# Kernel tuning notes

Hardware: AMD Instinct MI355X
Metric: run time of the kernel (lower is better)

Reference implementation:

```python
import jax, jax.numpy as jnp
import numpy as np

D_MODEL = 1024
N_HEADS = 16
FEATURE_DIM = 16
HEAD_DIM = D_MODEL // N_HEADS  # 64
EPS = 1e-12


def taylor_exp(x):
    """2nd-order Taylor feature map of exp(q^T k / sqrt(d)).
    x: (b, h, l, d) -> (b, h, l, 1 + d + d^2)"""
    d = x.shape[-1]
    rd = jnp.sqrt(jnp.asarray(d, x.dtype))      # sqrt(d)
    rrd = jnp.sqrt(rd)                          # d^(1/4)
    r2 = jnp.sqrt(jnp.asarray(2.0, x.dtype))
    x2 = (x[..., :, None] * x[..., None, :]).reshape(*x.shape[:-1], d * d) / r2
    ones = jnp.ones_like(x[..., :1])
    return jnp.concatenate([ones, x / rrd, x2 / rd], axis=-1)


def setup_inputs() -> dict:
    key = jax.random.key(0)
    k0, k1, k2, k3, k4 = jax.random.split(key, 5)
    b, l = 1, 1024
    scale = 1.0 / np.sqrt(D_MODEL)
    hidden_states = jax.random.normal(k0, (b, l, D_MODEL), dtype=jnp.float32)
    Wq = jax.random.normal(k1, (N_HEADS * FEATURE_DIM, D_MODEL), dtype=jnp.float32) * scale
    Wk = jax.random.normal(k2, (N_HEADS * FEATURE_DIM, D_MODEL), dtype=jnp.float32) * scale
    Wv = jax.random.normal(k3, (N_HEADS * HEAD_DIM, D_MODEL), dtype=jnp.float32) * scale
    Wo = jax.random.normal(k4, (D_MODEL, N_HEADS * HEAD_DIM), dtype=jnp.float32) * scale
    return {"hidden_states": hidden_states, "Wq": Wq, "Wk": Wk, "Wv": Wv, "Wo": Wo}


def reference(hidden_states, Wq, Wk, Wv, Wo):
    b, l, _ = hidden_states.shape
    # projections (bias-free)
    q = (hidden_states @ Wq.T).reshape(b, l, N_HEADS, FEATURE_DIM).transpose(0, 2, 1, 3)
    k = (hidden_states @ Wk.T).reshape(b, l, N_HEADS, FEATURE_DIM).transpose(0, 2, 1, 3)
    v = (hidden_states @ Wv.T).reshape(b, l, N_HEADS, HEAD_DIM).transpose(0, 2, 1, 3)
    qf = taylor_exp(q)   # (b, h, l, D) with D = 1 + d + d^2 = 273
    kf = taylor_exp(k)
    # causal linear attention via associative KV accumulation
    # kv_state[l] = sum_{t<=l} phi(k_t) outer v_t  -> (b, h, l, head_dim, D)
    kv_state = jnp.cumsum(kf[..., None, :] * v[..., :, None], axis=2)
    num = jnp.einsum('bhlD,bhldD->bhld', qf, kv_state)
    den = jnp.einsum('bhlD,bhlD->bhl', qf, jnp.cumsum(kf, axis=2))[..., None] + EPS
    y = num / den                                # (b, h, l, head_dim)
    y = y.transpose(0, 2, 1, 3).reshape(b, l, N_HEADS * HEAD_DIM)
    return y @ Wo.T
```

## Files before the change

kernel.cpp:

```cpp
#include <hip/hip_runtime.h>

#define LSEQ 1024
#define DMODEL 1024
#define NHEADS 16
#define FDIM 16
#define HDIM 64
#define CHUNK 64
#define NCHUNK 16

typedef __attribute__((ext_vector_type(8))) short short8;
typedef __attribute__((ext_vector_type(4))) float floatx4;

__device__ __forceinline__ float bf2f(unsigned short u) {
    unsigned int x = ((unsigned int)u) << 16;
    return __builtin_bit_cast(float, x);
}
__device__ __forceinline__ unsigned short f2bf(float f) {
    unsigned int x = __builtin_bit_cast(unsigned int, f);
    unsigned int r = (x + 0x7fffu + ((x >> 16) & 1u)) >> 16;
    return (unsigned short)r;
}

__device__ __forceinline__ int block_detect_fp32(const unsigned short* wq) {
    __shared__ int cnt;
    if (threadIdx.x == 0) cnt = 0;
    __syncthreads();
    int bad = 0;
    for (int i = threadIdx.x; i < 1024; i += blockDim.x) {
        int e = (wq[i] >> 7) & 0xFF;
        if (e >= 143 || (e > 0 && e <= 80)) bad++;
    }
    if (bad) atomicAdd(&cnt, bad);
    __syncthreads();
    return cnt > 128;
}

#define U_QB   0
#define U_KB   262144
#define U_VB   524288
#define U_YB   1572864
#define U_END  2621440

#define MFMA(a, b, c) __builtin_amdgcn_mfma_f32_16x16x32_bf16((a), (b), (c), 0, 0, 0)

__device__ __forceinline__ void gemm64_body(
    unsigned short (&As)[64][136], unsigned short (&Bs)[64][136],
    const void* Araw, int a_fp32, int arow0,
    const void* Braw, int b_fp32, int brow0, floatx4 acc[4]) {
    int t = threadIdx.x;
    int r = t >> 2, c0 = (t & 3) * 32;
    int wave = t >> 6, lane = t & 63;
    int ml = lane & 15, q4 = lane >> 4;
    int mq = (wave >> 1) * 32, nq = (wave & 1) * 32;
    #pragma unroll
    for (int i = 0; i < 4; ++i) acc[i] = (floatx4){0.f, 0.f, 0.f, 0.f};

    short8 av[4], bv[4], av2[4], bv2[4];
    auto stage = [&](int k0, short8* a, short8* b) {
        if (!a_fp32) {
            const unsigned short* Ap = (const unsigned short*)Araw + (size_t)(arow0 + r) * DMODEL + k0 + c0;
            #pragma unroll
            for (int j = 0; j < 4; ++j) a[j] = *(const short8*)(Ap + j * 8);
        } else {
            const float* Ap = (const float*)Araw + (size_t)(arow0 + r) * DMODEL + k0 + c0;
            #pragma unroll
            for (int j = 0; j < 4; ++j) {
                float4 f0 = *(const float4*)(Ap + j * 8);
                float4 f1 = *(const float4*)(Ap + j * 8 + 4);
                short8 x;
                x[0] = (short)f2bf(f0.x); x[1] = (short)f2bf(f0.y);
                x[2] = (short)f2bf(f0.z); x[3] = (short)f2bf(f0.w);
                x[4] = (short)f2bf(f1.x); x[5] = (short)f2bf(f1.y);
                x[6] = (short)f2bf(f1.z); x[7] = (short)f2bf(f1.w);
                a[j] = x;
            }
        }
        if (!b_fp32) {
            const unsigned short* Bp = (const unsigned short*)Braw + (size_t)(brow0 + r) * DMODEL + k0 + c0;
            #pragma unroll
            for (int j = 0; j < 4; ++j) b[j] = *(const short8*)(Bp + j * 8);
        } else {
            const float* Bp = (const float*)Braw + (size_t)(brow0 + r) * DMODEL + k0 + c0;
            #pragma unroll
            for (int j = 0; j < 4; ++j) {
                float4 f0 = *(const float4*)(Bp + j * 8);
                float4 f1 = *(const float4*)(Bp + j * 8 + 4);
                short8 x;
                x[0] = (short)f2bf(f0.x); x[1] = (short)f2bf(f0.y);
                x[2] = (short)f2bf(f0.z); x[3] = (short)f2bf(f0.w);
                x[4] = (short)f2bf(f1.x); x[5] = (short)f2bf(f1.y);
                x[6] = (short)f2bf(f1.z); x[7] = (short)f2bf(f1.w);
                b[j] = x;
            }
        }
    };

    stage(0, av, bv);
    for (int k0 = 0; k0 < DMODEL; k0 += 128) {
        __syncthreads();
        #pragma unroll
        for (int j = 0; j < 4; ++j) {
            *(short8*)&As[r][c0 + j * 8] = av[j];
            *(short8*)&Bs[r][c0 + j * 8] = bv[j];
        }
        __syncthreads();
        if (k0 + 128 < DMODEL) stage(k0 + 128, av2, bv2);
        #pragma unroll
        for (int kk = 0; kk < 4; ++kk) {
            short8 a0 = *(const short8*)&As[mq + ml][kk * 32 + q4 * 8];
            short8 a1 = *(const short8*)&As[mq + 16 + ml][kk * 32 + q4 * 8];
            short8 b0 = *(const short8*)&Bs[nq + ml][kk * 32 + q4 * 8];
            short8 b1 = *(const short8*)&Bs[nq + 16 + ml][kk * 32 + q4 * 8];
            acc[0] = MFMA(a0, b0, acc[0]); acc[1] = MFMA(a0, b1, acc[1]);
            acc[2] = MFMA(a1, b0, acc[2]); acc[3] = MFMA(a1, b1, acc[3]);
        }
        #pragma unroll
        for (int j = 0; j < 4; ++j) { av[j] = av2[j]; bv[j] = bv2[j]; }
    }
}

__global__ __launch_bounds__(256) void qkv_gemm(
    const void* __restrict__ hidR, const void* __restrict__ WqR,
    const void* __restrict__ WkR, const void* __restrict__ WvR,
    unsigned short* __restrict__ qb, unsigned short* __restrict__ kb,
    unsigned short* __restrict__ vb) {
    int fp32 = block_detect_fp32((const unsigned short*)WqR);
    __shared__ __align__(16) unsigned short As[64][136];
    __shared__ __align__(16) unsigned short Bs[64][136];
    int nb = blockIdx.x, mb = blockIdx.y;
    const void* Braw; unsigned short* Cout; int ldc, col0, br0;
    if (nb < 4)      { Braw = WqR; br0 = nb * 64;       Cout = qb; ldc = 256;  col0 = nb * 64; }
    else if (nb < 8) { Braw = WkR; br0 = (nb - 4) * 64; Cout = kb; ldc = 256;  col0 = (nb - 4) * 64; }
    else             { Braw = WvR; br0 = (nb - 8) * 64; Cout = vb; ldc = 1024; col0 = (nb - 8) * 64; }

    floatx4 acc[4];
    gemm64_body(As, Bs, hidR, fp32, mb * 64, Braw, fp32, br0, acc);

    int wave = threadIdx.x >> 6, lane = threadIdx.x & 63;
    int ml = lane & 15, q4 = lane >> 4;
    int mq = (wave >> 1) * 32, nq = (wave & 1) * 32;
    #pragma unroll
    for (int mi = 0; mi < 2; ++mi)
        #pragma unroll
        for (int ni = 0; ni < 2; ++ni) {
            floatx4 a = acc[mi * 2 + ni];
            int nloc = nq + ni * 16 + ml;
            #pragma unroll
            for (int r4 = 0; r4 < 4; ++r4) {
                int row = mb * 64 + mq + mi * 16 + q4 * 4 + r4;
                Cout[(size_t)row * ldc + col0 + nloc] = f2bf(a[r4]);
            }
        }
}

__global__ __launch_bounds__(256) void flash_partial(
    const unsigned short* __restrict__ qb, const unsigned short* __restrict__ kb,
    const unsigned short* __restrict__ vb,
    float* __restrict__ numW, float* __restrict__ denW) {
    int idx = blockIdx.x & 255;
    int s = blockIdx.x >> 8;
    int h = idx & 15, c = idx >> 4;
    int half = (c + 1) >> 1;
    int j0 = s ? half : 0;
    int j1 = s ? c : half - 1;
    int l0 = c * CHUNK;
    __shared__ __align__(16) unsigned short qs[64][40];
    __shared__ __align__(16) unsigned short ksm[64][40];
    __shared__ __align__(16) unsigned short vT[80][72];
    __shared__ __align__(16) unsigned short P[64][72];
    int t = threadIdx.x, lane = t & 63, wave = t >> 6;
    int ml = lane & 15, q4 = lane >> 4;
    int m0 = wave * 16;
    int sm = t >> 2, si4 = (t & 3) * 4, scc = (t & 3) * 16;

    {
        *(ushort4*)&qs[sm][si4] = *(const ushort4*)&qb[(size_t)(l0 + sm) * 256 + h * 16 + si4];
        ushort4 z = {0, 0, 0, 0};
        *(ushort4*)&qs[sm][16 + si4]  = z;
        *(ushort4*)&ksm[sm][16 + si4] = z;
    }
    if (t < 64) {
        vT[64][t] = 0x3F80;
        #pragma unroll
        for (int i = 65; i < 80; ++i) vT[i][t] = 0;
    }

    auto load_kv = [&](int j, ushort4& kr, ushort4 vr[4]) {
        kr = *(const ushort4*)&kb[(size_t)(j * 64 + sm) * 256 + h * 16 + si4];
        #pragma unroll
        for (int u = 0; u < 4; ++u)
            vr[u] = *(const ushort4*)&vb[(size_t)(j * 64 + sm) * 1024 + h * 64 + scc + u * 4];
    };

    floatx4 acc[5];
    #pragma unroll
    for (int i = 0; i < 5; ++i) acc[i] = (floatx4){0.f, 0.f, 0.f, 0.f};

    ushort4 kr, vr[4], kr2, vr2[4];
    if (j0 <= j1) {
        load_kv(j0, kr, vr);
        for (int j = j0; j <= j1; ++j) {
            {
                *(ushort4*)&ksm[sm][si4] = kr;
                unsigned short tmp[16];
                #pragma unroll
                for (int u = 0; u < 4; ++u) *(ushort4*)&tmp[u * 4] = vr[u];
                #pragma unroll
                for (int u = 0; u < 16; ++u) vT[scc + u][sm] = tmp[u];
            }
            __syncthreads();
            if (j < j1) load_kv(j + 1, kr2, vr2);

            short8 aq = *(const short8*)&qs[m0 + ml][q4 * 8];
            bool diag = (j == c);
            #pragma unroll
            for (int nt = 0; nt < 4; ++nt) {
                short8 bk = *(const short8*)&ksm[nt * 16 + ml][q4 * 8];
                floatx4 s4 = {0.f, 0.f, 0.f, 0.f};
                s4 = MFMA(aq, bk, s4);
                int tt = nt * 16 + ml;
                #pragma unroll
                for (int r = 0; r < 4; ++r) {
                    int lrow = m0 + q4 * 4 + r;
                    float sc = s4[r];
                    float p = 1.f + 0.25f * sc + 0.03125f * sc * sc;
                    if (diag && tt > lrow) p = 0.f;
                    P[lrow][tt] = f2bf(p);
                }
            }

            #pragma unroll
            for (int k0 = 0; k0 < 64; k0 += 32) {
                short8 ap = *(const short8*)&P[m0 + ml][k0 + q4 * 8];
                #pragma unroll
                for (int nt = 0; nt < 5; ++nt) {
                    short8 bvv = *(const short8*)&vT[nt * 16 + ml][k0 + q4 * 8];
                    acc[nt] = MFMA(ap, bvv, acc[nt]);
                }
            }
            __syncthreads();
            kr = kr2;
            #pragma unroll
            for (int u = 0; u < 4; ++u) vr[u] = vr2[u];
        }
    }

    float* np = numW + ((size_t)idx * 2 + s) * 4096;
    #pragma unroll
    for (int nt = 0; nt < 4; ++nt)
        #pragma unroll
        for (int r = 0; r < 4; ++r)
            np[(m0 + q4 * 4 + r) * 64 + nt * 16 + ml] = acc[nt][r];
    if (ml == 0) {
        float* dp = denW + ((size_t)idx * 2 + s) * 64;
        #pragma unroll
        for (int r = 0; r < 4; ++r) dp[m0 + q4 * 4 + r] = acc[4][r];
    }
}

__global__ __launch_bounds__(256) void attn_combine(
    const float* __restrict__ numW, const float* __restrict__ denW,
    unsigned short* __restrict__ ybB) {
    int idx = blockIdx.x;
    int h = idx & 15, c = idx >> 4;
    int l0 = c * CHUNK;
    int t = threadIdx.x;
    int row = t >> 2, col0 = (t & 3) * 16;
    const float* n0 = numW + (size_t)idx * 2 * 4096 + row * 64 + col0;
    const float* n1 = n0 + 4096;
    const float* dp = denW + (size_t)idx * 2 * 64 + row;
    float den = dp[0] + dp[64] + 1e-12f;
    float dinv = 1.f / den;
    short8 o0, o1;
    #pragma unroll
    for (int u = 0; u < 8; ++u)  o0[u] = (short)f2bf((n0[u] + n1[u]) * dinv);
    #pragma unroll
    for (int u = 8; u < 16; ++u) o1[u - 8] = (short)f2bf((n0[u] + n1[u]) * dinv);
    unsigned short* yp = ybB + (size_t)(l0 + row) * 1024 + h * 64 + col0;
    *(short8*)yp       = o0;
    *(short8*)(yp + 8) = o1;
}

__global__ __launch_bounds__(256) void out_gemm(
    const unsigned short* __restrict__ A, const void* __restrict__ WoR,
    void* __restrict__ outv, const unsigned short* __restrict__ wqraw) {
    int fp32 = block_detect_fp32(wqraw);
    __shared__ __align__(16) unsigned short As[64][136];
    __shared__ __align__(16) unsigned short Bs[64][136];
    int nb = blockIdx.x, mb = blockIdx.y;

    floatx4 acc[4];
    gemm64_body(As, Bs, A, 0, mb * 64, WoR, fp32, nb * 64, acc);

    int wave = threadIdx.x >> 6, lane = threadIdx.x & 63;
    int ml = lane & 15, q4 = lane >> 4;
    int mq = (wave >> 1) * 32, nq = (wave & 1) * 32;
    #pragma unroll
    for (int mi = 0; mi < 2; ++mi)
        #pragma unroll
        for (int ni = 0; ni < 2; ++ni) {
            floatx4 a = acc[mi * 2 + ni];
            int n = nb * 64 + nq + ni * 16 + ml;
            #pragma unroll
            for (int r4 = 0; r4 < 4; ++r4) {
                int row = mb * 64 + mq + mi * 16 + q4 * 4 + r4;
                size_t idx = (size_t)row * 1024 + n;
                if (fp32) ((float*)outv)[idx] = a[r4];
                else      ((unsigned short*)outv)[idx] = f2bf(a[r4]);
            }
        }
}

extern "C" void kernel_launch(void* const* d_in, const int* in_sizes, int n_in,
                              void* d_out, int out_size, void* d_ws, size_t ws_size,
                              hipStream_t stream) {
    unsigned short* us = (unsigned short*)d_ws;
    unsigned short* qbB = us + U_QB;
    unsigned short* kbB = us + U_KB;
    unsigned short* vbB = us + U_VB;
    unsigned short* ybB = us + U_YB;
    float* fws  = (float*)(us + U_END);
    float* numW = fws;
    float* denW = fws + 2097152;
    size_t need = (size_t)U_END * 2ull + (size_t)(2097152 + 32768) * 4ull;
    if (ws_size < need) return;

    qkv_gemm<<<dim3(24, 16), 256, 0, stream>>>(d_in[0], d_in[1], d_in[2], d_in[3], qbB, kbB, vbB);
    flash_partial<<<dim3(512), 256, 0, stream>>>(qbB, kbB, vbB, numW, denW);
    attn_combine<<<dim3(256), 256, 0, stream>>>(numW, denW, ybB);
    out_gemm<<<dim3(16, 16), 256, 0, stream>>>(ybB, d_in[4], d_out, (const unsigned short*)d_in[1]);
}
```

Before: 140.0 us.

## Fuse attention combine into output GEMM and store V transposed

Removes the attn_combine kernel. The output GEMM now reads the two partial numerator and denominator buffers directly, normalizes them, converts to bf16 and stages them into its A tile. The QKV GEMM writes V transposed, so flash_partial can load it with vector loads instead of scattering a transpose into shared memory. The PV MFMA operands are swapped so accumulator results can be written out as float4, and the bf16 conversion now uses the native __bf16 cast. The trade-off is that the output GEMM reads fp32 partials twice over (16 column blocks each reread them) instead of a single bf16 Y buffer.

```diff
diff --git a/kernel.cpp b/kernel.cpp
--- a/kernel.cpp
+++ b/kernel.cpp
@@ -11,14 +11,8 @@
 typedef __attribute__((ext_vector_type(8))) short short8;
 typedef __attribute__((ext_vector_type(4))) float floatx4;
 
-__device__ __forceinline__ float bf2f(unsigned short u) {
-    unsigned int x = ((unsigned int)u) << 16;
-    return __builtin_bit_cast(float, x);
-}
 __device__ __forceinline__ unsigned short f2bf(float f) {
-    unsigned int x = __builtin_bit_cast(unsigned int, f);
-    unsigned int r = (x + 0x7fffu + ((x >> 16) & 1u)) >> 16;
-    return (unsigned short)r;
+    return __builtin_bit_cast(unsigned short, (__bf16)f);
 }
 
 __device__ __forceinline__ int block_detect_fp32(const unsigned short* wq) {
@@ -37,8 +31,7 @@
 
 #define U_QB   0
 #define U_KB   262144
-#define U_VB   524288
-#define U_YB   1572864
+#define U_VT   524288
 #define U_END  2621440
 
 #define MFMA(a, b, c) __builtin_amdgcn_mfma_f32_16x16x32_bf16((a), (b), (c), 0, 0, 0)
@@ -56,6 +49,14 @@
     for (int i = 0; i < 4; ++i) acc[i] = (floatx4){0.f, 0.f, 0.f, 0.f};
 
     short8 av[4], bv[4], av2[4], bv2[4];
+    auto cvt8 = [](float4 f0, float4 f1) {
+        short8 x;
+        x[0] = (short)f2bf(f0.x); x[1] = (short)f2bf(f0.y);
+        x[2] = (short)f2bf(f0.z); x[3] = (short)f2bf(f0.w);
+        x[4] = (short)f2bf(f1.x); x[5] = (short)f2bf(f1.y);
+        x[6] = (short)f2bf(f1.z); x[7] = (short)f2bf(f1.w);
+        return x;
+    };
     auto stage = [&](int k0, short8* a, short8* b) {
         if (!a_fp32) {
             const unsigned short* Ap = (const unsigned short*)Araw + (size_t)(arow0 + r) * DMODEL + k0 + c0;
@@ -64,16 +65,8 @@
         } else {
             const float* Ap = (const float*)Araw + (size_t)(arow0 + r) * DMODEL + k0 + c0;
             #pragma unroll
-            for (int j = 0; j < 4; ++j) {
-                float4 f0 = *(const float4*)(Ap + j * 8);
-                float4 f1 = *(const float4*)(Ap + j * 8 + 4);
-                short8 x;
-                x[0] = (short)f2bf(f0.x); x[1] = (short)f2bf(f0.y);
-                x[2] = (short)f2bf(f0.z); x[3] = (short)f2bf(f0.w);
-                x[4] = (short)f2bf(f1.x); x[5] = (short)f2bf(f1.y);
-                x[6] = (short)f2bf(f1.z); x[7] = (short)f2bf(f1.w);
-                a[j] = x;
-            }
+            for (int j = 0; j < 4; ++j)
+                a[j] = cvt8(*(const float4*)(Ap + j * 8), *(const float4*)(Ap + j * 8 + 4));
         }
         if (!b_fp32) {
             const unsigned short* Bp = (const unsigned short*)Braw + (size_t)(brow0 + r) * DMODEL + k0 + c0;
@@ -82,16 +75,8 @@
         } else {
             const float* Bp = (const float*)Braw + (size_t)(brow0 + r) * DMODEL + k0 + c0;
             #pragma unroll
-            for (int j = 0; j < 4; ++j) {
-                float4 f0 = *(const float4*)(Bp + j * 8);
-                float4 f1 = *(const float4*)(Bp + j * 8 + 4);
-                short8 x;
-                x[0] = (short)f2bf(f0.x); x[1] = (short)f2bf(f0.y);
-                x[2] = (short)f2bf(f0.z); x[3] = (short)f2bf(f0.w);
-                x[4] = (short)f2bf(f1.x); x[5] = (short)f2bf(f1.y);
-                x[6] = (short)f2bf(f1.z); x[7] = (short)f2bf(f1.w);
-                b[j] = x;
-            }
+            for (int j = 0; j < 4; ++j)
+                b[j] = cvt8(*(const float4*)(Bp + j * 8), *(const float4*)(Bp + j * 8 + 4));
         }
     };
 
@@ -123,15 +108,15 @@
     const void* __restrict__ hidR, const void* __restrict__ WqR,
     const void* __restrict__ WkR, const void* __restrict__ WvR,
     unsigned short* __restrict__ qb, unsigned short* __restrict__ kb,
-    unsigned short* __restrict__ vb) {
+    unsigned short* __restrict__ vt) {
     int fp32 = block_detect_fp32((const unsigned short*)WqR);
     __shared__ __align__(16) unsigned short As[64][136];
     __shared__ __align__(16) unsigned short Bs[64][136];
     int nb = blockIdx.x, mb = blockIdx.y;
-    const void* Braw; unsigned short* Cout; int ldc, col0, br0;
-    if (nb < 4)      { Braw = WqR; br0 = nb * 64;       Cout = qb; ldc = 256;  col0 = nb * 64; }
-    else if (nb < 8) { Braw = WkR; br0 = (nb - 4) * 64; Cout = kb; ldc = 256;  col0 = (nb - 4) * 64; }
-    else             { Braw = WvR; br0 = (nb - 8) * 64; Cout = vb; ldc = 1024; col0 = (nb - 8) * 64; }
+    const void* Braw; unsigned short* Cout; int ldc, col0, br0, isv;
+    if (nb < 4)      { Braw = WqR; br0 = nb * 64;       Cout = qb; ldc = 256;  col0 = nb * 64;       isv = 0; }
+    else if (nb < 8) { Braw = WkR; br0 = (nb - 4) * 64; Cout = kb; ldc = 256;  col0 = (nb - 4) * 64; isv = 0; }
+    else             { Braw = WvR; br0 = (nb - 8) * 64; Cout = vt; ldc = 0;    col0 = (nb - 8) * 64; isv = 1; }
 
     floatx4 acc[4];
     gemm64_body(As, Bs, hidR, fp32, mb * 64, Braw, fp32, br0, acc);
@@ -139,23 +124,38 @@
     int wave = threadIdx.x >> 6, lane = threadIdx.x & 63;
     int ml = lane & 15, q4 = lane >> 4;
     int mq = (wave >> 1) * 32, nq = (wave & 1) * 32;
-    #pragma unroll
-    for (int mi = 0; mi < 2; ++mi)
-        #pragma unroll
-        for (int ni = 0; ni < 2; ++ni) {
-            floatx4 a = acc[mi * 2 + ni];
-            int nloc = nq + ni * 16 + ml;
-            #pragma unroll
-            for (int r4 = 0; r4 < 4; ++r4) {
-                int row = mb * 64 + mq + mi * 16 + q4 * 4 + r4;
-                Cout[(size_t)row * ldc + col0 + nloc] = f2bf(a[r4]);
-            }
-        }
+    if (!isv) {
+        #pragma unroll
+        for (int mi = 0; mi < 2; ++mi)
+            #pragma unroll
+            for (int ni = 0; ni < 2; ++ni) {
+                floatx4 a = acc[mi * 2 + ni];
+                int nloc = nq + ni * 16 + ml;
+                #pragma unroll
+                for (int r4 = 0; r4 < 4; ++r4) {
+                    int row = mb * 64 + mq + mi * 16 + q4 * 4 + r4;
+                    Cout[(size_t)row * ldc + col0 + nloc] = f2bf(a[r4]);
+                }
+            }
+    } else {
+        #pragma unroll
+        for (int mi = 0; mi < 2; ++mi)
+            #pragma unroll
+            for (int ni = 0; ni < 2; ++ni) {
+                floatx4 a = acc[mi * 2 + ni];
+                int n = col0 + nq + ni * 16 + ml;
+                int row0 = mb * 64 + mq + mi * 16 + q4 * 4;
+                ushort4 o;
+                o.x = f2bf(a[0]); o.y = f2bf(a[1]);
+                o.z = f2bf(a[2]); o.w = f2bf(a[3]);
+                *(ushort4*)&vt[(size_t)n * 1024 + row0] = o;
+            }
+    }
 }
 
 __global__ __launch_bounds__(256) void flash_partial(
     const unsigned short* __restrict__ qb, const unsigned short* __restrict__ kb,
-    const unsigned short* __restrict__ vb,
+    const unsigned short* __restrict__ vt,
     float* __restrict__ numW, float* __restrict__ denW) {
     int idx = blockIdx.x & 255;
     int s = blockIdx.x >> 8;
@@ -171,7 +171,7 @@
     int t = threadIdx.x, lane = t & 63, wave = t >> 6;
     int ml = lane & 15, q4 = lane >> 4;
     int m0 = wave * 16;
-    int sm = t >> 2, si4 = (t & 3) * 4, scc = (t & 3) * 16;
+    int sm = t >> 2, si4 = (t & 3) * 4, sc16 = (t & 3) * 16;
 
     {
         *(ushort4*)&qs[sm][si4] = *(const ushort4*)&qb[(size_t)(l0 + sm) * 256 + h * 16 + si4];
@@ -185,31 +185,26 @@
         for (int i = 65; i < 80; ++i) vT[i][t] = 0;
     }
 
-    auto load_kv = [&](int j, ushort4& kr, ushort4 vr[4]) {
+    auto load_kv = [&](int j, ushort4& kr, short8& v0, short8& v1) {
         kr = *(const ushort4*)&kb[(size_t)(j * 64 + sm) * 256 + h * 16 + si4];
-        #pragma unroll
-        for (int u = 0; u < 4; ++u)
-            vr[u] = *(const ushort4*)&vb[(size_t)(j * 64 + sm) * 1024 + h * 64 + scc + u * 4];
+        const unsigned short* vp = vt + (size_t)(h * 64 + sm) * 1024 + j * 64 + sc16;
+        v0 = *(const short8*)vp;
+        v1 = *(const short8*)(vp + 8);
     };
 
     floatx4 acc[5];
     #pragma unroll
     for (int i = 0; i < 5; ++i) acc[i] = (floatx4){0.f, 0.f, 0.f, 0.f};
 
-    ushort4 kr, vr[4], kr2, vr2[4];
+    ushort4 kr, kr2; short8 va, vb2, va2, vb22;
     if (j0 <= j1) {
-        load_kv(j0, kr, vr);
+        load_kv(j0, kr, va, vb2);
         for (int j = j0; j <= j1; ++j) {
-            {
-                *(ushort4*)&ksm[sm][si4] = kr;
-                unsigned short tmp[16];
-                #pragma unroll
-                for (int u = 0; u < 4; ++u) *(ushort4*)&tmp[u * 4] = vr[u];
-                #pragma unroll
-                for (int u = 0; u < 16; ++u) vT[scc + u][sm] = tmp[u];
-            }
+            *(ushort4*)&ksm[sm][si4] = kr;
+            *(short8*)&vT[sm][sc16]     = va;
+            *(short8*)&vT[sm][sc16 + 8] = vb2;
             __syncthreads();
-            if (j < j1) load_kv(j + 1, kr2, vr2);
+            if (j < j1) load_kv(j + 1, kr2, va2, vb22);
 
             short8 aq = *(const short8*)&qs[m0 + ml][q4 * 8];
             bool diag = (j == c);
@@ -234,67 +229,106 @@
                 short8 ap = *(const short8*)&P[m0 + ml][k0 + q4 * 8];
                 #pragma unroll
                 for (int nt = 0; nt < 5; ++nt) {
-                    short8 bvv = *(const short8*)&vT[nt * 16 + ml][k0 + q4 * 8];
-                    acc[nt] = MFMA(ap, bvv, acc[nt]);
+                    short8 av = *(const short8*)&vT[nt * 16 + ml][k0 + q4 * 8];
+                    acc[nt] = MFMA(av, ap, acc[nt]);
                 }
             }
             __syncthreads();
-            kr = kr2;
-            #pragma unroll
-            for (int u = 0; u < 4; ++u) vr[u] = vr2[u];
-        }
-    }
-
-    float* np = numW + ((size_t)idx * 2 + s) * 4096;
+            kr = kr2; va = va2; vb2 = vb22;
+        }
+    }
+
+    float* np = numW + ((size_t)idx * 2 + s) * 4096 + (m0 + ml) * 64;
     #pragma unroll
     for (int nt = 0; nt < 4; ++nt)
-        #pragma unroll
-        for (int r = 0; r < 4; ++r)
-            np[(m0 + q4 * 4 + r) * 64 + nt * 16 + ml] = acc[nt][r];
-    if (ml == 0) {
-        float* dp = denW + ((size_t)idx * 2 + s) * 64;
-        #pragma unroll
-        for (int r = 0; r < 4; ++r) dp[m0 + q4 * 4 + r] = acc[4][r];
-    }
-}
-
-__global__ __launch_bounds__(256) void attn_combine(
+        *(floatx4*)&np[nt * 16 + q4 * 4] = acc[nt];
+    if (lane < 16) denW[((size_t)idx * 2 + s) * 64 + m0 + lane] = acc[4][0];
+}
+
+__global__ __launch_bounds__(256) void out_gemm(
     const float* __restrict__ numW, const float* __restrict__ denW,
-    unsigned short* __restrict__ ybB) {
-    int idx = blockIdx.x;
-    int h = idx & 15, c = idx >> 4;
-    int l0 = c * CHUNK;
-    int t = threadIdx.x;
-    int row = t >> 2, col0 = (t & 3) * 16;
-    const float* n0 = numW + (size_t)idx * 2 * 4096 + row * 64 + col0;
-    const float* n1 = n0 + 4096;
-    const float* dp = denW + (size_t)idx * 2 * 64 + row;
-    float den = dp[0] + dp[64] + 1e-12f;
-    float dinv = 1.f / den;
-    short8 o0, o1;
-    #pragma unroll
-    for (int u = 0; u < 8; ++u)  o0[u] = (short)f2bf((n0[u] + n1[u]) * dinv);
-    #pragma unroll
-    for (int u = 8; u < 16; ++u) o1[u - 8] = (short)f2bf((n0[u] + n1[u]) * dinv);
-    unsigned short* yp = ybB + (size_t)(l0 + row) * 1024 + h * 64 + col0;
-    *(short8*)yp       = o0;
-    *(short8*)(yp + 8) = o1;
-}
-
-__global__ __launch_bounds__(256) void out_gemm(
-    const unsigned short* __restrict__ A, const void* __restrict__ WoR,
-    void* __restrict__ outv, const unsigned short* __restrict__ wqraw) {
+    const void* __restrict__ WoR, void* __restrict__ outv,
+    const unsigned short* __restrict__ wqraw) {
     int fp32 = block_detect_fp32(wqraw);
     __shared__ __align__(16) unsigned short As[64][136];
     __shared__ __align__(16) unsigned short Bs[64][136];
     int nb = blockIdx.x, mb = blockIdx.y;
-
-    floatx4 acc[4];
-    gemm64_body(As, Bs, A, 0, mb * 64, WoR, fp32, nb * 64, acc);
-
-    int wave = threadIdx.x >> 6, lane = threadIdx.x & 63;
+    int t = threadIdx.x;
+    int r = t >> 2, c0 = (t & 3) * 32;
+    int wave = t >> 6, lane = t & 63;
     int ml = lane & 15, q4 = lane >> 4;
     int mq = (wave >> 1) * 32, nq = (wave & 1) * 32;
+    floatx4 acc[4];
+    #pragma unroll
+    for (int i = 0; i < 4; ++i) acc[i] = (floatx4){0.f, 0.f, 0.f, 0.f};
+
+    short8 av[4], bv[4], av2[4], bv2[4];
+    auto cvt8 = [](float4 f0, float4 f1) {
+        short8 x;
+        x[0] = (short)f2bf(f0.x); x[1] = (short)f2bf(f0.y);
+        x[2] = (short)f2bf(f0.z); x[3] = (short)f2bf(f0.w);
+        x[4] = (short)f2bf(f1.x); x[5] = (short)f2bf(f1.y);
+        x[6] = (short)f2bf(f1.z); x[7] = (short)f2bf(f1.w);
+        return x;
+    };
+    auto stageA = [&](int k0, short8* a) {
+        int kbase = k0 + c0;
+        int h = kbase >> 6;
+        size_t idx = (size_t)(mb * 16 + h);
+        const float* n0 = numW + idx * 2 * 4096 + r * 64 + (kbase & 63);
+        const float* n1 = n0 + 4096;
+        float den = denW[idx * 128 + r] + denW[idx * 128 + 64 + r] + 1e-12f;
+        float dinv = 1.f / den;
+        #pragma unroll
+        for (int j = 0; j < 4; ++j) {
+            float4 f0 = *(const float4*)(n0 + j * 8);
+            float4 f1 = *(const float4*)(n0 + j * 8 + 4);
+            float4 g0 = *(const float4*)(n1 + j * 8);
+            float4 g1 = *(const float4*)(n1 + j * 8 + 4);
+            float4 s0, s1;
+            s0.x = (f0.x + g0.x) * dinv; s0.y = (f0.y + g0.y) * dinv;
+            s0.z = (f0.z + g0.z) * dinv; s0.w = (f0.w + g0.w) * dinv;
+            s1.x = (f1.x + g1.x) * dinv; s1.y = (f1.y + g1.y) * dinv;
+            s1.z = (f1.z + g1.z) * dinv; s1.w = (f1.w + g1.w) * dinv;
+            a[j] = cvt8(s0, s1);
+        }
+    };
+    auto stageB = [&](int k0, short8* b) {
+        if (!fp32) {
+            const unsigned short* Bp = (const unsigned short*)WoR + (size_t)(nb * 64 + r) * DMODEL + k0 + c0;
+            #pragma unroll
+            for (int j = 0; j < 4; ++j) b[j] = *(const short8*)(Bp + j * 8);
+        } else {
+            const float* Bp = (const float*)WoR + (size_t)(nb * 64 + r) * DMODEL + k0 + c0;
+            #pragma unroll
+            for (int j = 0; j < 4; ++j)
+                b[j] = cvt8(*(const float4*)(Bp + j * 8), *(const float4*)(Bp + j * 8 + 4));
+        }
+    };
+
+    stageA(0, av); stageB(0, bv);
+    for (int k0 = 0; k0 < DMODEL; k0 += 128) {
+        __syncthreads();
+        #pragma unroll
+        for (int j = 0; j < 4; ++j) {
+            *(short8*)&As[r][c0 + j * 8] = av[j];
+            *(short8*)&Bs[r][c0 + j * 8] = bv[j];
+        }
+        __syncthreads();
+        if (k0 + 128 < DMODEL) { stageA(k0 + 128, av2); stageB(k0 + 128, bv2); }
+        #pragma unroll
+        for (int kk = 0; kk < 4; ++kk) {
+            short8 a0 = *(const short8*)&As[mq + ml][kk * 32 + q4 * 8];
+            short8 a1 = *(const short8*)&As[mq + 16 + ml][kk * 32 + q4 * 8];
+            short8 b0 = *(const short8*)&Bs[nq + ml][kk * 32 + q4 * 8];
+            short8 b1 = *(const short8*)&Bs[nq + 16 + ml][kk * 32 + q4 * 8];
+            acc[0] = MFMA(a0, b0, acc[0]); acc[1] = MFMA(a0, b1, acc[1]);
+            acc[2] = MFMA(a1, b0, acc[2]); acc[3] = MFMA(a1, b1, acc[3]);
+        }
+        #pragma unroll
+        for (int j = 0; j < 4; ++j) { av[j] = av2[j]; bv[j] = bv2[j]; }
+    }
+
     #pragma unroll
     for (int mi = 0; mi < 2; ++mi)
         #pragma unroll
@@ -304,9 +338,9 @@
             #pragma unroll
             for (int r4 = 0; r4 < 4; ++r4) {
                 int row = mb * 64 + mq + mi * 16 + q4 * 4 + r4;
-                size_t idx = (size_t)row * 1024 + n;
-                if (fp32) ((float*)outv)[idx] = a[r4];
-                else      ((unsigned short*)outv)[idx] = f2bf(a[r4]);
+                size_t oidx = (size_t)row * 1024 + n;
+                if (fp32) ((float*)outv)[oidx] = a[r4];
+                else      ((unsigned short*)outv)[oidx] = f2bf(a[r4]);
             }
         }
 }
@@ -317,16 +351,14 @@
     unsigned short* us = (unsigned short*)d_ws;
     unsigned short* qbB = us + U_QB;
     unsigned short* kbB = us + U_KB;
-    unsigned short* vbB = us + U_VB;
-    unsigned short* ybB = us + U_YB;
+    unsigned short* vtB = us + U_VT;
     float* fws  = (float*)(us + U_END);
     float* numW = fws;
     float* denW = fws + 2097152;
     size_t need = (size_t)U_END * 2ull + (size_t)(2097152 + 32768) * 4ull;
     if (ws_size < need) return;
 
-    qkv_gemm<<<dim3(24, 16), 256, 0, stream>>>(d_in[0], d_in[1], d_in[2], d_in[3], qbB, kbB, vbB);
-    flash_partial<<<dim3(512), 256, 0, stream>>>(qbB, kbB, vbB, numW, denW);
-    attn_combine<<<dim3(256), 256, 0, stream>>>(numW, denW, ybB);
-    out_gemm<<<dim3(16, 16), 256, 0, stream>>>(ybB, d_in[4], d_out, (const unsigned short*)d_in[1]);
-}
+    qkv_gemm<<<dim3(24, 16), 256, 0, stream>>>(d_in[0], d_in[1], d_in[2], d_in[3], qbB, kbB, vtB);
+    flash_partial<<<dim3(512), 256, 0, stream>>>(qbB, kbB, vtB, numW, denW);
+    out_gemm<<<dim3(16, 16), 256, 0, stream>>>(numW, denW, d_in[4], d_out, (const unsigned short*)d_in[1]);
+}
```

Measured after the change: 148.2 us. 1.06x slower.
